# Performance work log

Hardware: AMD Instinct MI355X
Metric: run time of the kernel (lower is better)

Reference implementation:

```python
import jax, jax.numpy as jnp
import numpy as np

S, N, C = 256, 512, 32   # n_seq, n_res, channels
EPS = 1e-3               # module eps for mask normalization
LN_EPS = 1e-5            # torch LayerNorm default eps


def setup_inputs() -> dict:
    key = jax.random.key(0)
    ks = jax.random.split(key, 6)
    scale = 1.0 / np.sqrt(C)
    return {
        "m": jax.random.normal(ks[0], (S, N, C), jnp.float32),
        "mask": jnp.ones((S, N), jnp.float32),
        "ln_gamma": jnp.ones((C,), jnp.float32),
        "ln_beta": jnp.zeros((C,), jnp.float32),
        "Wa": jax.random.normal(ks[1], (C, C), jnp.float32) * scale,
        "ba": jnp.zeros((C,), jnp.float32),
        "Wb": jax.random.normal(ks[2], (C, C), jnp.float32) * scale,
        "bb": jnp.zeros((C,), jnp.float32),
        "Wout": jax.random.normal(ks[3], (C * C, C), jnp.float32) * (1.0 / np.sqrt(C * C)),
        "bout": jnp.zeros((C,), jnp.float32),
    }


def reference(m, mask, ln_gamma, ln_beta, Wa, ba, Wb, bb, Wout, bout):
    # LayerNorm over channel dim
    mu = jnp.mean(m, axis=-1, keepdims=True)
    var = jnp.mean(jnp.square(m - mu), axis=-1, keepdims=True)
    mh = (m - mu) * jax.lax.rsqrt(var + LN_EPS) * ln_gamma + ln_beta  # [S, N, C]

    # dual linear projections, masked per (seq, res), then seq<->res transpose
    a = jnp.swapaxes((mh @ Wa + ba) * mask[..., None], -2, -3)  # [N, S, C]
    b = jnp.swapaxes((mh @ Wb + bb) * mask[..., None], -2, -3)  # [N, S, C]

    # outer product summed over sequences: [N, N, C, C] -> [N, N, C*C]
    outer = jnp.einsum("bac,dae->bdce", a, b).reshape(N, N, C * C)
    outer = outer @ Wout + bout  # [N, N, C]

    # pairwise mask normalization: sum over seqs of mask[s,i]*mask[s,j]
    norm = jnp.einsum("ab,ad->bd", mask, mask)[..., None] + EPS  # [N, N, 1]
    return outer / norm
```

## Files before the change

### kernel.cpp

```cpp
#include <hip/hip_runtime.h>

#define S_SEQ 256
#define N_RES 512
#define CCH   32

typedef __attribute__((ext_vector_type(8))) short bf16x8;
typedef __attribute__((ext_vector_type(4))) float f32x4;
typedef __attribute__((ext_vector_type(2))) unsigned int u32x2;

__device__ __forceinline__ unsigned short f2bf(float x) {
    unsigned int u = __float_as_uint(x);
    return (unsigned short)((u + 0x7FFFu + ((u >> 16) & 1u)) >> 16);
}

#define GLOAD_LDS16(gp, lp) __builtin_amdgcn_global_load_lds( \
    (const __attribute__((address_space(1))) unsigned int*)(gp), \
    (__attribute__((address_space(3))) unsigned int*)(lp), 16, 0, 0)

#define BAR()    do { __builtin_amdgcn_s_barrier(); asm volatile("" ::: "memory"); } while (0)
#define WLGKM0() asm volatile("s_waitcnt lgkmcnt(0)" ::: "memory")
#define WVM(n)   asm volatile("s_waitcnt vmcnt(" #n ")" ::: "memory")

__global__ __launch_bounds__(256) void prep_ab(
    const float* __restrict__ m, const float* __restrict__ mask,
    const float* __restrict__ gam, const float* __restrict__ bet,
    const float* __restrict__ Wa, const float* __restrict__ ba,
    const float* __restrict__ Wb, const float* __restrict__ bb,
    char* __restrict__ Ag, char* __restrict__ Bg)
{
    __shared__ float WaL[1024], WbL[1024];
    __shared__ float gL[32], btL[32], baL[32], bbL[32];
    __shared__ unsigned short At[32 * 256];
    __shared__ unsigned short Bt[32 * 256];

    const int n = blockIdx.x;
    const int t = threadIdx.x;

    for (int i = t; i < 1024; i += 256) { WaL[i] = Wa[i]; WbL[i] = Wb[i]; }
    if (t < 32) { gL[t] = gam[t]; btL[t] = bet[t]; baL[t] = ba[t]; bbL[t] = bb[t]; }
    __syncthreads();

    const int s = t;
    float mv[32];
    const float* mrow = m + ((size_t)s * N_RES + n) * CCH;
#pragma unroll
    for (int c4 = 0; c4 < 8; c4++) {
        f32x4 v = *(const f32x4*)(mrow + c4 * 4);
        mv[c4 * 4 + 0] = v.x; mv[c4 * 4 + 1] = v.y;
        mv[c4 * 4 + 2] = v.z; mv[c4 * 4 + 3] = v.w;
    }
    float mu = 0.f;
#pragma unroll
    for (int c = 0; c < 32; c++) mu += mv[c];
    mu *= (1.f / 32.f);
    float var = 0.f;
#pragma unroll
    for (int c = 0; c < 32; c++) { float d = mv[c] - mu; var += d * d; }
    var *= (1.f / 32.f);
    float rs = rsqrtf(var + 1e-5f);
    float mh[32];
#pragma unroll
    for (int c = 0; c < 32; c++) mh[c] = (mv[c] - mu) * rs * gL[c] + btL[c];

    const float msk = mask[(size_t)s * N_RES + n];

    f32x4 av[8], bv[8];
#pragma unroll
    for (int cg = 0; cg < 8; cg++) { av[cg] = (f32x4)0.f; bv[cg] = (f32x4)0.f; }
#pragma unroll
    for (int k = 0; k < 32; k++) {
        float x = mh[k];
#pragma unroll
        for (int cg = 0; cg < 8; cg++) {
            f32x4 wa4 = *(const f32x4*)&WaL[k * 32 + cg * 4];
            f32x4 wb4 = *(const f32x4*)&WbL[k * 32 + cg * 4];
            av[cg] += x * wa4;
            bv[cg] += x * wb4;
        }
    }
#pragma unroll
    for (int cg = 0; cg < 8; cg++) {
#pragma unroll
        for (int u = 0; u < 4; u++) {
            int c = cg * 4 + u;
            At[c * 256 + s] = f2bf((av[cg][u] + baL[c]) * msk);
            Bt[c * 256 + s] = f2bf((bv[cg][u] + bbL[c]) * msk);
        }
    }
    __syncthreads();

    const size_t tbase = (size_t)(n >> 3) * 131072;
    const int half = (n >> 2) & 1;
    const int irbase = (n & 3) * 32;
#pragma unroll
    for (int u = 0; u < 4; u++) {
        int cid = t * 4 + u;
        int c = cid >> 5, g = cid & 31;
        int kt = g >> 2, q = g & 3;
        int slot = ((half << 2) | q) ^ (c & 7);
        size_t off = tbase + (size_t)kt * 16384 + (size_t)(irbase + c) * 128 + (slot << 4);
        *(uint4*)(Ag + off) = *(const uint4*)(At + c * 256 + g * 8);
        *(uint4*)(Bg + off) = *(const uint4*)(Bt + c * 256 + g * 8);
    }
}

__global__ __launch_bounds__(256) void kwt(const float* __restrict__ Wout,
                                           unsigned short* __restrict__ Wt3)
{
    int idx = blockIdx.x * 256 + threadIdx.x;
    int e = idx >> 10, ch = (idx >> 5) & 31, c = idx & 31;
    Wt3[idx] = f2bf(Wout[(size_t)(c * 32 + e) * 32 + ch]);
}

__global__ __launch_bounds__(256) void knorm(const float* __restrict__ mask,
                                             float* __restrict__ inv_norm)
{
    __shared__ float Mi[64][65];
    __shared__ float Mj[64][65];
    const int bi = blockIdx.x >> 3, bj = blockIdx.x & 7;
    const int t = threadIdx.x;
    const int ty = t >> 4, tx = t & 15;

    float acc[4][4];
#pragma unroll
    for (int a = 0; a < 4; a++)
#pragma unroll
        for (int b = 0; b < 4; b++) acc[a][b] = 0.f;

    for (int sc = 0; sc < 4; sc++) {
        for (int e = t; e < 4096; e += 256) {
            int sr = e >> 6, col = e & 63;
            Mi[sr][col] = mask[(size_t)(sc * 64 + sr) * N_RES + bi * 64 + col];
            Mj[sr][col] = mask[(size_t)(sc * 64 + sr) * N_RES + bj * 64 + col];
        }
        __syncthreads();
        for (int sp = 0; sp < 64; sp++) {
#pragma unroll
            for (int a = 0; a < 4; a++)
#pragma unroll
                for (int b = 0; b < 4; b++)
                    acc[a][b] += Mi[sp][ty * 4 + a] * Mj[sp][tx * 4 + b];
        }
        __syncthreads();
    }
#pragma unroll
    for (int a = 0; a < 4; a++)
#pragma unroll
        for (int b = 0; b < 4; b++) {
            int i = bi * 64 + ty * 4 + a;
            int j = bj * 64 + tx * 4 + b;
            inv_norm[(size_t)i * N_RES + j] = 1.f / (acc[a][b] + 1e-3f);
        }
}

__global__ __launch_bounds__(512) void kmain5(
    const char* __restrict__ Ag, const char* __restrict__ Bg,
    const unsigned short* __restrict__ Wt3, const float* __restrict__ inv_norm,
    const float* __restrict__ bout, float* __restrict__ out)
{
    __shared__ __align__(16) char sm[98304];

    const int bid = blockIdx.x;
    const int xcd = bid & 7;
    const int xidx = bid >> 3;
    const int chunk = xidx >> 7;
    const int TI = xcd * 8 + ((xidx >> 4) & 7);
    const int TJ = chunk * 16 + (xidx & 15);

    const int t = threadIdx.x;
    const int lane = t & 63, wid = t >> 6;
    const int wr = wid >> 2, wc = wid & 3;
    const int rl = lane & 15, h4 = lane >> 4;

    const char* pa = Ag + (size_t)TI * 131072;
    const char* pb = Bg + (size_t)TJ * 131072;

#define SH(kt) do { \
    char* db_ = sm + (((kt) % 3) * 32768); \
    GLOAD_LDS16(pa + (kt) * 16384 + t * 16,        db_ + t * 16); \
    GLOAD_LDS16(pa + (kt) * 16384 + 8192 + t * 16, db_ + 8192 + t * 16); \
    GLOAD_LDS16(pb + (kt) * 16384 + t * 16,        db_ + 16384 + t * 16); \
    GLOAD_LDS16(pb + (kt) * 16384 + 8192 + t * 16, db_ + 24576 + t * 16); \
} while (0)

    const int aslot = ((wr << 2) | h4) ^ (rl & 7);
    const int bslot = (((wc >> 1) << 2) | h4) ^ (rl & 7);
    const int abase = rl * 128 + (aslot << 4);
    const int bbase = 16384 + ((wc & 1) * 64 + rl) * 128 + (bslot << 4);

    f32x4 acc[8][4];
#pragma unroll
    for (int a = 0; a < 8; a++)
#pragma unroll
        for (int b = 0; b < 4; b++) acc[a][b] = (f32x4)0.f;

    SH(0);
    SH(1);

#pragma unroll
    for (int kt = 0; kt < 8; kt++) {
        const char* buf = sm + ((kt % 3) * 32768);
        if (kt < 7) { WVM(4); } else { WVM(0); }
        WLGKM0();
        BAR();
        if (kt < 6) SH(kt + 2);
        bf16x8 af[8], bfr[4];
#pragma unroll
        for (int am = 0; am < 8; am++)
            af[am] = *(const bf16x8*)(buf + abase + am * 2048);
#pragma unroll
        for (int bn = 0; bn < 4; bn++)
            bfr[bn] = *(const bf16x8*)(buf + bbase + bn * 2048);
        __builtin_amdgcn_s_setprio(1);
#pragma unroll
        for (int am = 0; am < 8; am++)
#pragma unroll
            for (int bn = 0; bn < 4; bn++)
                acc[am][bn] = __builtin_amdgcn_mfma_f32_16x16x32_bf16(
                    af[am], bfr[bn], acc[am][bn], 0, 0, 0);
        __builtin_amdgcn_s_setprio(0);
    }
#undef SH

    WLGKM0();
    BAR();

    float* ps = (float*)sm;
#pragma unroll
    for (int R = 0; R < 2; R++) {
#pragma unroll
        for (int a = 0; a < 4; a++) {
            const int am = R * 4 + a;
            const int lpr = ((a >> 1) & 1) * 8 + wc * 2;
            const int cs = ((a & 1) << 1) + (h4 >> 1);
#pragma unroll
            for (int bn = 0; bn < 4; bn++) {
                const int lp = lpr + (bn >> 1);
                const int e = ((bn & 1) << 4) + rl;
                unsigned int lo = (unsigned int)f2bf(acc[am][bn][0]) |
                                  ((unsigned int)f2bf(acc[am][bn][1]) << 16);
                unsigned int hi = (unsigned int)f2bf(acc[am][bn][2]) |
                                  ((unsigned int)f2bf(acc[am][bn][3]) << 16);
                u32x2 wv; wv[0] = lo; wv[1] = hi;
                *(u32x2*)(sm + wr * 33024 + lp * 2064 + e * 64 +
                          ((cs ^ (e & 3)) << 4) + ((h4 & 1) << 3)) = wv;
            }
        }
        WLGKM0();
        BAR();
        const int slotR = wid >> 2, kq = wid & 3;
        f32x4 ae0 = (f32x4)0.f, ae1 = (f32x4)0.f;
        const char* grow = sm + slotR * 33024 + rl * 2064;
#pragma unroll
        for (int es = 0; es < 8; es++) {
            const int e = kq * 8 + es;
            bf16x8 ga = *(const bf16x8*)(grow + e * 64 + ((h4 ^ (e & 3)) << 4));
            bf16x8 wb0 = *(const bf16x8*)(Wt3 + (size_t)e * 1024 + rl * 32 + h4 * 8);
            bf16x8 wb1 = *(const bf16x8*)(Wt3 + (size_t)e * 1024 + (16 + rl) * 32 + h4 * 8);
            ae0 = __builtin_amdgcn_mfma_f32_16x16x32_bf16(ga, wb0, ae0, 0, 0, 0);
            ae1 = __builtin_amdgcn_mfma_f32_16x16x32_bf16(ga, wb1, ae1, 0, 0, 0);
        }
        WLGKM0();
        BAR();
#pragma unroll
        for (int r = 0; r < 4; r++) {
            ps[((slotR * 4 + kq) * 16 + h4 * 4 + r) * 34 + rl]      = ae0[r];
            ps[((slotR * 4 + kq) * 16 + h4 * 4 + r) * 34 + 16 + rl] = ae1[r];
        }
        WLGKM0();
        BAR();
#pragma unroll
        for (int u = 0; u < 2; u++) {
            const int lp = (t >> 5) & 15, ch = t & 31;
            float v = 0.f;
#pragma unroll
            for (int k2 = 0; k2 < 4; k2++)
                v += ps[((u * 4 + k2) * 16 + lp) * 34 + ch];
            const int pi = u * 4 + R * 2 + (lp >> 3), pj = lp & 7;
            const int i = TI * 8 + pi, j = TJ * 8 + pj;
            out[((size_t)(i * N_RES + j)) * CCH + ch] =
                (v + bout[ch]) * inv_norm[(size_t)i * N_RES + j];
        }
        BAR();
    }
}

extern "C" void kernel_launch(void* const* d_in, const int* in_sizes, int n_in,
                              void* d_out, int out_size, void* d_ws, size_t ws_size,
                              hipStream_t stream)
{
    const float* m    = (const float*)d_in[0];
    const float* mask = (const float*)d_in[1];
    const float* gam  = (const float*)d_in[2];
    const float* bet  = (const float*)d_in[3];
    const float* Wa   = (const float*)d_in[4];
    const float* ba   = (const float*)d_in[5];
    const float* Wb   = (const float*)d_in[6];
    const float* bb   = (const float*)d_in[7];
    const float* Wout = (const float*)d_in[8];
    const float* bout = (const float*)d_in[9];
    float* out = (float*)d_out;

    char* ws = (char*)d_ws;
    char* Ag = ws;
    char* Bg = ws + 8388608;
    unsigned short* Wt3 = (unsigned short*)(ws + 16777216);
    float* inv_norm = (float*)(ws + 16842752);

    prep_ab<<<dim3(N_RES), dim3(256), 0, stream>>>(m, mask, gam, bet, Wa, ba, Wb, bb, Ag, Bg);
    kwt<<<dim3(128), dim3(256), 0, stream>>>(Wout, Wt3);
    knorm<<<dim3(64), dim3(256), 0, stream>>>(mask, inv_norm);
    kmain5<<<dim3(4096), dim3(512), 0, stream>>>(Ag, Bg, Wt3, inv_norm, bout, out);
}
```

Baseline: 241.3 us.

## Restructure main GEMM loop into double-buffered 64-wide k-tiles with sub-phase scheduling

```diff
diff --git a/kernel.cpp b/kernel.cpp
--- a/kernel.cpp
+++ b/kernel.cpp
@@ -153,12 +153,12 @@
         }
 }
 
-__global__ __launch_bounds__(512) void kmain5(
+__global__ __launch_bounds__(512, 2) void kmain6(
     const char* __restrict__ Ag, const char* __restrict__ Bg,
     const unsigned short* __restrict__ Wt3, const float* __restrict__ inv_norm,
     const float* __restrict__ bout, float* __restrict__ out)
 {
-    __shared__ __align__(16) char sm[98304];
+    __shared__ __align__(16) char sm[131072];
 
     const int bid = blockIdx.x;
     const int xcd = bid & 7;
@@ -175,18 +175,65 @@
     const char* pa = Ag + (size_t)TI * 131072;
     const char* pb = Bg + (size_t)TJ * 131072;
 
-#define SH(kt) do { \
-    char* db_ = sm + (((kt) % 3) * 32768); \
-    GLOAD_LDS16(pa + (kt) * 16384 + t * 16,        db_ + t * 16); \
-    GLOAD_LDS16(pa + (kt) * 16384 + 8192 + t * 16, db_ + 8192 + t * 16); \
-    GLOAD_LDS16(pb + (kt) * 16384 + t * 16,        db_ + 16384 + t * 16); \
-    GLOAD_LDS16(pb + (kt) * 16384 + 8192 + t * 16, db_ + 24576 + t * 16); \
-} while (0)
-
     const int aslot = ((wr << 2) | h4) ^ (rl & 7);
     const int bslot = (((wc >> 1) << 2) | h4) ^ (rl & 7);
     const int abase = rl * 128 + (aslot << 4);
-    const int bbase = 16384 + ((wc & 1) * 64 + rl) * 128 + (bslot << 4);
+    const int bbase = ((wc & 1) * 64 + rl) * 128 + (bslot << 4);
+
+#define SCH(T1, c) GLOAD_LDS16( \
+    (((c) < 4) ? pa : pb) + (T1) * 32768 + ((c) & 3) * 8192 + t * 16, \
+    sm + (((T1) & 1) * 65536) + (((c) < 4) ? 0 : 32768) + ((c) & 3) * 8192 + t * 16)
+
+#define FRAG_A(dst, bufc, k, MB) do { \
+    _Pragma("unroll") \
+    for (int mm = 0; mm < 4; mm++) \
+        dst[mm] = *(const bf16x8*)((bufc) + (k) * 16384 + abase + ((MB) + mm) * 2048); \
+} while (0)
+
+#define FRAG_B(dst, bufc, k) do { \
+    _Pragma("unroll") \
+    for (int nn = 0; nn < 4; nn++) \
+        dst[nn] = *(const bf16x8*)((bufc) + 32768 + (k) * 16384 + bbase + nn * 2048); \
+} while (0)
+
+#define MFMA16(A4, B4, MB) do { \
+    __builtin_amdgcn_s_setprio(1); \
+    _Pragma("unroll") \
+    for (int mm = 0; mm < 4; mm++) \
+        _Pragma("unroll") \
+        for (int nn = 0; nn < 4; nn++) \
+            acc[(MB) + mm][nn] = __builtin_amdgcn_mfma_f32_16x16x32_bf16( \
+                A4[mm], B4[nn], acc[(MB) + mm][nn], 0, 0, 0); \
+    __builtin_amdgcn_s_setprio(0); \
+} while (0)
+
+#define KTILE(T) do { \
+    const char* bufc = sm + (((T) & 1) * 65536); \
+    bf16x8 a0[4], a1[4], b0[4], b1[4]; \
+     \
+    FRAG_A(a0, bufc, 0, 0); FRAG_B(b0, bufc, 0); \
+    if ((T) < 3) { SCH((T)+1, 0); SCH((T)+1, 1); SCH((T)+1, 4); SCH((T)+1, 5); } \
+    BAR(); WLGKM0(); \
+    MFMA16(a0, b0, 0); \
+    BAR(); \
+     \
+    FRAG_A(a1, bufc, 0, 4); FRAG_B(b1, bufc, 1); \
+    if ((T) < 3) { SCH((T)+1, 2); SCH((T)+1, 3); SCH((T)+1, 6); SCH((T)+1, 7); } \
+    BAR(); WLGKM0(); \
+    MFMA16(a1, b0, 4); \
+    BAR(); \
+     \
+    FRAG_A(a0, bufc, 1, 0); \
+    BAR(); WLGKM0(); \
+    MFMA16(a0, b1, 0); \
+    BAR(); \
+     \
+    FRAG_A(a1, bufc, 1, 4); \
+    BAR(); WLGKM0(); \
+    MFMA16(a1, b1, 4); \
+    if ((T) < 3) { WVM(0); } \
+    BAR(); \
+} while (0)
 
     f32x4 acc[8][4];
 #pragma unroll
@@ -194,36 +241,21 @@
 #pragma unroll
         for (int b = 0; b < 4; b++) acc[a][b] = (f32x4)0.f;
 
-    SH(0);
-    SH(1);
-
-#pragma unroll
-    for (int kt = 0; kt < 8; kt++) {
-        const char* buf = sm + ((kt % 3) * 32768);
-        if (kt < 7) { WVM(4); } else { WVM(0); }
-        WLGKM0();
-        BAR();
-        if (kt < 6) SH(kt + 2);
-        bf16x8 af[8], bfr[4];
-#pragma unroll
-        for (int am = 0; am < 8; am++)
-            af[am] = *(const bf16x8*)(buf + abase + am * 2048);
-#pragma unroll
-        for (int bn = 0; bn < 4; bn++)
-            bfr[bn] = *(const bf16x8*)(buf + bbase + bn * 2048);
-        __builtin_amdgcn_s_setprio(1);
-#pragma unroll
-        for (int am = 0; am < 8; am++)
-#pragma unroll
-            for (int bn = 0; bn < 4; bn++)
-                acc[am][bn] = __builtin_amdgcn_mfma_f32_16x16x32_bf16(
-                    af[am], bfr[bn], acc[am][bn], 0, 0, 0);
-        __builtin_amdgcn_s_setprio(0);
-    }
-#undef SH
-
-    WLGKM0();
+#pragma unroll
+    for (int c = 0; c < 8; c++) SCH(0, c);
+    WVM(0);
     BAR();
+
+    KTILE(0);
+    KTILE(1);
+    KTILE(2);
+    KTILE(3);
+
+#undef KTILE
+#undef MFMA16
+#undef FRAG_A
+#undef FRAG_B
+#undef SCH
 
     float* ps = (float*)sm;
 #pragma unroll
@@ -310,5 +342,5 @@
     prep_ab<<<dim3(N_RES), dim3(256), 0, stream>>>(m, mask, gam, bet, Wa, ba, Wb, bb, Ag, Bg);
     kwt<<<dim3(128), dim3(256), 0, stream>>>(Wout, Wt3);
     knorm<<<dim3(64), dim3(256), 0, stream>>>(mask, inv_norm);
-    kmain5<<<dim3(4096), dim3(512), 0, stream>>>(Ag, Bg, Wt3, inv_norm, bout, out);
-}
+    kmain6<<<dim3(4096), dim3(512), 0, stream>>>(Ag, Bg, Wt3, inv_norm, bout, out);
+}
```

Measured after the change: 252.4 us. 1.05x slower.

## Halve A tile per block, double-buffer LDS, raise occupancy in outer-product kernel

Applied to the files above, without the earlier changes.

```diff
diff --git a/kernel.cpp b/kernel.cpp
--- a/kernel.cpp
+++ b/kernel.cpp
@@ -89,18 +89,22 @@
     }
     __syncthreads();
 
-    const size_t tbase = (size_t)(n >> 3) * 131072;
-    const int half = (n >> 2) & 1;
-    const int irbase = (n & 3) * 32;
+    const size_t taA = (size_t)(n >> 2) * 65536;
+    const size_t taB = (size_t)(n >> 3) * 131072;
+    const int irb = (n & 3) * 32;
+    const int halfB = (n >> 2) & 1;
 #pragma unroll
     for (int u = 0; u < 4; u++) {
         int cid = t * 4 + u;
         int c = cid >> 5, g = cid & 31;
         int kt = g >> 2, q = g & 3;
-        int slot = ((half << 2) | q) ^ (c & 7);
-        size_t off = tbase + (size_t)kt * 16384 + (size_t)(irbase + c) * 128 + (slot << 4);
-        *(uint4*)(Ag + off) = *(const uint4*)(At + c * 256 + g * 8);
-        *(uint4*)(Bg + off) = *(const uint4*)(Bt + c * 256 + g * 8);
+        size_t offA = taA + (size_t)kt * 8192
+                    + (size_t)(irb + c) * 64 + (size_t)((q ^ (c & 3)) << 4);
+        size_t offB = taB + (size_t)kt * 16384
+                    + (size_t)(irb + c) * 128
+                    + (size_t)((((halfB << 2) | q) ^ (c & 7)) << 4);
+        *(uint4*)(Ag + offA) = *(const uint4*)(At + c * 256 + g * 8);
+        *(uint4*)(Bg + offB) = *(const uint4*)(Bt + c * 256 + g * 8);
     }
 }
 
@@ -153,18 +157,18 @@
         }
 }
 
-__global__ __launch_bounds__(512) void kmain5(
+__global__ __launch_bounds__(512, 4) void kmain7(
     const char* __restrict__ Ag, const char* __restrict__ Bg,
     const unsigned short* __restrict__ Wt3, const float* __restrict__ inv_norm,
     const float* __restrict__ bout, float* __restrict__ out)
 {
-    __shared__ __align__(16) char sm[98304];
+    __shared__ __align__(16) char sm[66048];
 
     const int bid = blockIdx.x;
     const int xcd = bid & 7;
     const int xidx = bid >> 3;
-    const int chunk = xidx >> 7;
-    const int TI = xcd * 8 + ((xidx >> 4) & 7);
+    const int chunk = xidx >> 8;
+    const int TI = xcd * 16 + ((xidx >> 4) & 15);
     const int TJ = chunk * 16 + (xidx & 15);
 
     const int t = threadIdx.x;
@@ -172,25 +176,23 @@
     const int wr = wid >> 2, wc = wid & 3;
     const int rl = lane & 15, h4 = lane >> 4;
 
-    const char* pa = Ag + (size_t)TI * 131072;
+    const char* pa = Ag + (size_t)TI * 65536;
     const char* pb = Bg + (size_t)TJ * 131072;
 
 #define SH(kt) do { \
-    char* db_ = sm + (((kt) % 3) * 32768); \
-    GLOAD_LDS16(pa + (kt) * 16384 + t * 16,        db_ + t * 16); \
-    GLOAD_LDS16(pa + (kt) * 16384 + 8192 + t * 16, db_ + 8192 + t * 16); \
-    GLOAD_LDS16(pb + (kt) * 16384 + t * 16,        db_ + 16384 + t * 16); \
-    GLOAD_LDS16(pb + (kt) * 16384 + 8192 + t * 16, db_ + 24576 + t * 16); \
+    char* db_ = sm + (((kt) & 1) * 24576); \
+    GLOAD_LDS16(pa + (kt) * 8192 + t * 16,         db_ + t * 16); \
+    GLOAD_LDS16(pb + (kt) * 16384 + t * 16,        db_ + 8192 + t * 16); \
+    GLOAD_LDS16(pb + (kt) * 16384 + 8192 + t * 16, db_ + 16384 + t * 16); \
 } while (0)
 
-    const int aslot = ((wr << 2) | h4) ^ (rl & 7);
-    const int bslot = (((wc >> 1) << 2) | h4) ^ (rl & 7);
-    const int abase = rl * 128 + (aslot << 4);
-    const int bbase = 16384 + ((wc & 1) * 64 + rl) * 128 + (bslot << 4);
-
-    f32x4 acc[8][4];
-#pragma unroll
-    for (int a = 0; a < 8; a++)
+    const int abase = (wr * 64 + rl) * 64 + ((h4 ^ (rl & 3)) << 4);
+    const int bbase = 8192 + ((wc & 1) * 64 + rl) * 128
+                    + (((((wc >> 1) << 2) | h4) ^ (rl & 7)) << 4);
+
+    f32x4 acc[4][4];
+#pragma unroll
+    for (int a = 0; a < 4; a++)
 #pragma unroll
         for (int b = 0; b < 4; b++) acc[a][b] = (f32x4)0.f;
 
@@ -199,89 +201,85 @@
 
 #pragma unroll
     for (int kt = 0; kt < 8; kt++) {
-        const char* buf = sm + ((kt % 3) * 32768);
-        if (kt < 7) { WVM(4); } else { WVM(0); }
-        WLGKM0();
+        if (kt < 7) { WVM(3); } else { WVM(0); }
         BAR();
-        if (kt < 6) SH(kt + 2);
-        bf16x8 af[8], bfr[4];
-#pragma unroll
-        for (int am = 0; am < 8; am++)
-            af[am] = *(const bf16x8*)(buf + abase + am * 2048);
+        const char* buf = sm + ((kt & 1) * 24576);
+        bf16x8 af[4], bfr[4];
+#pragma unroll
+        for (int am = 0; am < 4; am++)
+            af[am] = *(const bf16x8*)(buf + abase + am * 1024);
 #pragma unroll
         for (int bn = 0; bn < 4; bn++)
             bfr[bn] = *(const bf16x8*)(buf + bbase + bn * 2048);
+        WLGKM0();
         __builtin_amdgcn_s_setprio(1);
 #pragma unroll
-        for (int am = 0; am < 8; am++)
+        for (int am = 0; am < 4; am++)
 #pragma unroll
             for (int bn = 0; bn < 4; bn++)
                 acc[am][bn] = __builtin_amdgcn_mfma_f32_16x16x32_bf16(
                     af[am], bfr[bn], acc[am][bn], 0, 0, 0);
         __builtin_amdgcn_s_setprio(0);
+        BAR();
+        if (kt <= 5) SH(kt + 2);
     }
 #undef SH
 
+#pragma unroll
+    for (int am = 0; am < 4; am++) {
+        const int lpr = (am >> 1) * 8 + wc * 2;
+        const int cs = ((am & 1) << 1) + (h4 >> 1);
+#pragma unroll
+        for (int bn = 0; bn < 4; bn++) {
+            const int lp = lpr + (bn >> 1);
+            const int e = ((bn & 1) << 4) + rl;
+            unsigned int lo = (unsigned int)f2bf(acc[am][bn][0]) |
+                              ((unsigned int)f2bf(acc[am][bn][1]) << 16);
+            unsigned int hi = (unsigned int)f2bf(acc[am][bn][2]) |
+                              ((unsigned int)f2bf(acc[am][bn][3]) << 16);
+            u32x2 wv; wv[0] = lo; wv[1] = hi;
+            *(u32x2*)(sm + wr * 33024 + lp * 2064 + e * 64 +
+                      ((cs ^ (e & 3)) << 4) + ((h4 & 1) << 3)) = wv;
+        }
+    }
     WLGKM0();
     BAR();
 
+    const int slotR = wid >> 2, kq = wid & 3;
+    f32x4 ae0 = (f32x4)0.f, ae1 = (f32x4)0.f;
+    const char* grow = sm + slotR * 33024 + rl * 2064;
+#pragma unroll
+    for (int es = 0; es < 8; es++) {
+        const int e = kq * 8 + es;
+        bf16x8 ga = *(const bf16x8*)(grow + e * 64 + ((h4 ^ (e & 3)) << 4));
+        bf16x8 wb0 = *(const bf16x8*)(Wt3 + (size_t)e * 1024 + rl * 32 + h4 * 8);
+        bf16x8 wb1 = *(const bf16x8*)(Wt3 + (size_t)e * 1024 + (16 + rl) * 32 + h4 * 8);
+        ae0 = __builtin_amdgcn_mfma_f32_16x16x32_bf16(ga, wb0, ae0, 0, 0, 0);
+        ae1 = __builtin_amdgcn_mfma_f32_16x16x32_bf16(ga, wb1, ae1, 0, 0, 0);
+    }
+    WLGKM0();
+    BAR();
+
     float* ps = (float*)sm;
 #pragma unroll
-    for (int R = 0; R < 2; R++) {
-#pragma unroll
-        for (int a = 0; a < 4; a++) {
-            const int am = R * 4 + a;
-            const int lpr = ((a >> 1) & 1) * 8 + wc * 2;
-            const int cs = ((a & 1) << 1) + (h4 >> 1);
-#pragma unroll
-            for (int bn = 0; bn < 4; bn++) {
-                const int lp = lpr + (bn >> 1);
-                const int e = ((bn & 1) << 4) + rl;
-                unsigned int lo = (unsigned int)f2bf(acc[am][bn][0]) |
-                                  ((unsigned int)f2bf(acc[am][bn][1]) << 16);
-                unsigned int hi = (unsigned int)f2bf(acc[am][bn][2]) |
-                                  ((unsigned int)f2bf(acc[am][bn][3]) << 16);
-                u32x2 wv; wv[0] = lo; wv[1] = hi;
-                *(u32x2*)(sm + wr * 33024 + lp * 2064 + e * 64 +
-                          ((cs ^ (e & 3)) << 4) + ((h4 & 1) << 3)) = wv;
-            }
-        }
-        WLGKM0();
-        BAR();
-        const int slotR = wid >> 2, kq = wid & 3;
-        f32x4 ae0 = (f32x4)0.f, ae1 = (f32x4)0.f;
-        const char* grow = sm + slotR * 33024 + rl * 2064;
-#pragma unroll
-        for (int es = 0; es < 8; es++) {
-            const int e = kq * 8 + es;
-            bf16x8 ga = *(const bf16x8*)(grow + e * 64 + ((h4 ^ (e & 3)) << 4));
-            bf16x8 wb0 = *(const bf16x8*)(Wt3 + (size_t)e * 1024 + rl * 32 + h4 * 8);
-            bf16x8 wb1 = *(const bf16x8*)(Wt3 + (size_t)e * 1024 + (16 + rl) * 32 + h4 * 8);
-            ae0 = __builtin_amdgcn_mfma_f32_16x16x32_bf16(ga, wb0, ae0, 0, 0, 0);
-            ae1 = __builtin_amdgcn_mfma_f32_16x16x32_bf16(ga, wb1, ae1, 0, 0, 0);
-        }
-        WLGKM0();
-        BAR();
-#pragma unroll
-        for (int r = 0; r < 4; r++) {
-            ps[((slotR * 4 + kq) * 16 + h4 * 4 + r) * 34 + rl]      = ae0[r];
-            ps[((slotR * 4 + kq) * 16 + h4 * 4 + r) * 34 + 16 + rl] = ae1[r];
-        }
-        WLGKM0();
-        BAR();
-#pragma unroll
-        for (int u = 0; u < 2; u++) {
-            const int lp = (t >> 5) & 15, ch = t & 31;
-            float v = 0.f;
-#pragma unroll
-            for (int k2 = 0; k2 < 4; k2++)
-                v += ps[((u * 4 + k2) * 16 + lp) * 34 + ch];
-            const int pi = u * 4 + R * 2 + (lp >> 3), pj = lp & 7;
-            const int i = TI * 8 + pi, j = TJ * 8 + pj;
-            out[((size_t)(i * N_RES + j)) * CCH + ch] =
-                (v + bout[ch]) * inv_norm[(size_t)i * N_RES + j];
-        }
-        BAR();
+    for (int r = 0; r < 4; r++) {
+        ps[((slotR * 4 + kq) * 16 + h4 * 4 + r) * 34 + rl]      = ae0[r];
+        ps[((slotR * 4 + kq) * 16 + h4 * 4 + r) * 34 + 16 + rl] = ae1[r];
+    }
+    WLGKM0();
+    BAR();
+
+#pragma unroll
+    for (int u = 0; u < 2; u++) {
+        const int idx = u * 512 + t;
+        const int p = idx >> 5, ch = idx & 31;
+        float v = 0.f;
+#pragma unroll
+        for (int k2 = 0; k2 < 4; k2++)
+            v += ps[(((p >> 4) * 4 + k2) * 16 + (p & 15)) * 34 + ch];
+        const int i = TI * 4 + (p >> 3), j = TJ * 8 + (p & 7);
+        out[((size_t)(i * N_RES + j)) * CCH + ch] =
+            (v + bout[ch]) * inv_norm[(size_t)i * N_RES + j];
     }
 }
 
@@ -310,5 +308,5 @@
     prep_ab<<<dim3(N_RES), dim3(256), 0, stream>>>(m, mask, gam, bet, Wa, ba, Wb, bb, Ag, Bg);
     kwt<<<dim3(128), dim3(256), 0, stream>>>(Wout, Wt3);
     knorm<<<dim3(64), dim3(256), 0, stream>>>(mask, inv_norm);
-    kmain5<<<dim3(4096), dim3(512), 0, stream>>>(Ag, Bg, Wt3, inv_norm, bout, out);
-}
+    kmain7<<<dim3(8192), dim3(512), 0, stream>>>(Ag, Bg, Wt3, inv_norm, bout, out);
+}
```

Measured after the change: 210.4 us. 12.8% less time.

## Shrink LDS to double buffer for two blocks per CU, use packed bf16 convert

Applied to the files above, without the earlier changes.

```diff
diff --git a/kernel.cpp b/kernel.cpp
--- a/kernel.cpp
+++ b/kernel.cpp
@@ -11,6 +11,12 @@
 __device__ __forceinline__ unsigned short f2bf(float x) {
     unsigned int u = __float_as_uint(x);
     return (unsigned short)((u + 0x7FFFu + ((u >> 16) & 1u)) >> 16);
+}
+
+__device__ __forceinline__ unsigned int cvtpk(float lo, float hi) {
+    unsigned int r;
+    asm("v_cvt_pk_bf16_f32 %0, %1, %2" : "=v"(r) : "v"(lo), "v"(hi));
+    return r;
 }
 
 #define GLOAD_LDS16(gp, lp) __builtin_amdgcn_global_load_lds( \
@@ -153,19 +159,18 @@
         }
 }
 
-__global__ __launch_bounds__(512) void kmain5(
+__global__ __launch_bounds__(512, 2) void kmain10(
     const char* __restrict__ Ag, const char* __restrict__ Bg,
     const unsigned short* __restrict__ Wt3, const float* __restrict__ inv_norm,
     const float* __restrict__ bout, float* __restrict__ out)
 {
-    __shared__ __align__(16) char sm[98304];
+    __shared__ __align__(16) char sm[66048];
 
     const int bid = blockIdx.x;
     const int xcd = bid & 7;
     const int xidx = bid >> 3;
-    const int chunk = xidx >> 7;
     const int TI = xcd * 8 + ((xidx >> 4) & 7);
-    const int TJ = chunk * 16 + (xidx & 15);
+    const int TJ = (xidx >> 7) * 16 + (xidx & 15);
 
     const int t = threadIdx.x;
     const int lane = t & 63, wid = t >> 6;
@@ -176,17 +181,16 @@
     const char* pb = Bg + (size_t)TJ * 131072;
 
 #define SH(kt) do { \
-    char* db_ = sm + (((kt) % 3) * 32768); \
+    char* db_ = sm + (((kt) & 1) * 32768); \
     GLOAD_LDS16(pa + (kt) * 16384 + t * 16,        db_ + t * 16); \
     GLOAD_LDS16(pa + (kt) * 16384 + 8192 + t * 16, db_ + 8192 + t * 16); \
     GLOAD_LDS16(pb + (kt) * 16384 + t * 16,        db_ + 16384 + t * 16); \
     GLOAD_LDS16(pb + (kt) * 16384 + 8192 + t * 16, db_ + 24576 + t * 16); \
 } while (0)
 
-    const int aslot = ((wr << 2) | h4) ^ (rl & 7);
-    const int bslot = (((wc >> 1) << 2) | h4) ^ (rl & 7);
-    const int abase = rl * 128 + (aslot << 4);
-    const int bbase = 16384 + ((wc & 1) * 64 + rl) * 128 + (bslot << 4);
+    const int abase = rl * 128 + ((((wr << 2) | h4) ^ (rl & 7)) << 4);
+    const int bbase = 16384 + ((wc & 1) * 64 + rl) * 128
+                    + (((((wc >> 1) << 2) | h4) ^ (rl & 7)) << 4);
 
     f32x4 acc[8][4];
 #pragma unroll
@@ -199,11 +203,9 @@
 
 #pragma unroll
     for (int kt = 0; kt < 8; kt++) {
-        const char* buf = sm + ((kt % 3) * 32768);
         if (kt < 7) { WVM(4); } else { WVM(0); }
-        WLGKM0();
-        BAR();
-        if (kt < 6) SH(kt + 2);
+        BAR();
+        const char* buf = sm + ((kt & 1) * 32768);
         bf16x8 af[8], bfr[4];
 #pragma unroll
         for (int am = 0; am < 8; am++)
@@ -219,11 +221,10 @@
                 acc[am][bn] = __builtin_amdgcn_mfma_f32_16x16x32_bf16(
                     af[am], bfr[bn], acc[am][bn], 0, 0, 0);
         __builtin_amdgcn_s_setprio(0);
+        BAR();
+        if (kt <= 5) SH(kt + 2);
     }
 #undef SH
-
-    WLGKM0();
-    BAR();
 
     float* ps = (float*)sm;
 #pragma unroll
@@ -231,36 +232,33 @@
 #pragma unroll
         for (int a = 0; a < 4; a++) {
             const int am = R * 4 + a;
-            const int lpr = ((a >> 1) & 1) * 8 + wc * 2;
+            const int lpr = (wr * 2 + (a >> 1)) * 8 + wc * 2;
             const int cs = ((a & 1) << 1) + (h4 >> 1);
 #pragma unroll
             for (int bn = 0; bn < 4; bn++) {
                 const int lp = lpr + (bn >> 1);
                 const int e = ((bn & 1) << 4) + rl;
-                unsigned int lo = (unsigned int)f2bf(acc[am][bn][0]) |
-                                  ((unsigned int)f2bf(acc[am][bn][1]) << 16);
-                unsigned int hi = (unsigned int)f2bf(acc[am][bn][2]) |
-                                  ((unsigned int)f2bf(acc[am][bn][3]) << 16);
-                u32x2 wv; wv[0] = lo; wv[1] = hi;
-                *(u32x2*)(sm + wr * 33024 + lp * 2064 + e * 64 +
-                          ((cs ^ (e & 3)) << 4) + ((h4 & 1) << 3)) = wv;
+                u32x2 wv;
+                wv[0] = cvtpk(acc[am][bn][0], acc[am][bn][1]);
+                wv[1] = cvtpk(acc[am][bn][2], acc[am][bn][3]);
+                *(u32x2*)(sm + lp * 2064 + e * 64 +
+                          ((cs ^ ((e >> 1) & 3)) << 4) + ((h4 & 1) << 3)) = wv;
             }
         }
         WLGKM0();
         BAR();
         const int slotR = wid >> 2, kq = wid & 3;
         f32x4 ae0 = (f32x4)0.f, ae1 = (f32x4)0.f;
-        const char* grow = sm + slotR * 33024 + rl * 2064;
+        const char* grow = sm + (slotR * 16 + rl) * 2064;
 #pragma unroll
         for (int es = 0; es < 8; es++) {
             const int e = kq * 8 + es;
-            bf16x8 ga = *(const bf16x8*)(grow + e * 64 + ((h4 ^ (e & 3)) << 4));
+            bf16x8 ga = *(const bf16x8*)(grow + e * 64 + ((h4 ^ ((e >> 1) & 3)) << 4));
             bf16x8 wb0 = *(const bf16x8*)(Wt3 + (size_t)e * 1024 + rl * 32 + h4 * 8);
             bf16x8 wb1 = *(const bf16x8*)(Wt3 + (size_t)e * 1024 + (16 + rl) * 32 + h4 * 8);
             ae0 = __builtin_amdgcn_mfma_f32_16x16x32_bf16(ga, wb0, ae0, 0, 0, 0);
             ae1 = __builtin_amdgcn_mfma_f32_16x16x32_bf16(ga, wb1, ae1, 0, 0, 0);
         }
-        WLGKM0();
         BAR();
 #pragma unroll
         for (int r = 0; r < 4; r++) {
@@ -271,12 +269,15 @@
         BAR();
 #pragma unroll
         for (int u = 0; u < 2; u++) {
-            const int lp = (t >> 5) & 15, ch = t & 31;
+            const int idx = u * 512 + t;
+            const int lp = idx >> 5, ch = idx & 31;
             float v = 0.f;
 #pragma unroll
             for (int k2 = 0; k2 < 4; k2++)
-                v += ps[((u * 4 + k2) * 16 + lp) * 34 + ch];
-            const int pi = u * 4 + R * 2 + (lp >> 3), pj = lp & 7;
+                v += ps[(((lp >> 4) * 4 + k2) * 16 + (lp & 15)) * 34 + ch];
+            const int lr = lp >> 3;
+            const int pi = (lr >> 1) * 4 + 2 * R + (lr & 1);
+            const int pj = lp & 7;
             const int i = TI * 8 + pi, j = TJ * 8 + pj;
             out[((size_t)(i * N_RES + j)) * CCH + ch] =
                 (v + bout[ch]) * inv_norm[(size_t)i * N_RES + j];
@@ -310,5 +311,5 @@
     prep_ab<<<dim3(N_RES), dim3(256), 0, stream>>>(m, mask, gam, bet, Wa, ba, Wb, bb, Ag, Bg);
     kwt<<<dim3(128), dim3(256), 0, stream>>>(Wout, Wt3);
     knorm<<<dim3(64), dim3(256), 0, stream>>>(mask, inv_norm);
-    kmain5<<<dim3(4096), dim3(512), 0, stream>>>(Ag, Bg, Wt3, inv_norm, bout, out);
-}
+    kmain10<<<dim3(4096), dim3(512), 0, stream>>>(Ag, Bg, Wt3, inv_norm, bout, out);
+}
```

Measured after the change: 233.8 us. 1.03x faster.
